# Optimization experiments

Hardware: AMD Instinct MI355X
Metric: run time of the kernel (lower is better)

Reference implementation:

```python
import jax, jax.numpy as jnp
import numpy as np
import math

B, T, C, H = 16384, 64, 48, 48


def setup_inputs() -> dict:
    key = jax.random.key(0)
    kx, kq, kk, kv = jax.random.split(key, 4)
    return {
        "x": jax.random.normal(kx, (B, T, C), dtype=jnp.float32),
        "Wq": jax.random.normal(kq, (C, H), dtype=jnp.float32) * 0.02,
        "Wk": jax.random.normal(kk, (C, H), dtype=jnp.float32) * 0.02,
        "Wv": jax.random.normal(kv, (C, H), dtype=jnp.float32) * 0.02,
    }


def reference(x, Wq, Wk, Wv):
    # x: [B, T, C]; projections (Linear with bias=False): [B, T, H]
    q = x @ Wq
    k = x @ Wk
    v = x @ Wv
    scale = 1.0 / math.sqrt(H)
    # scores: [B, T, T]
    wei = jnp.einsum("bth,bsh->bts", q, k) * scale
    causal = jnp.tril(jnp.ones((T, T), dtype=bool))  # tril mask, T==BLOCK_SIZE
    wei = jnp.where(causal, wei, -jnp.inf)
    wei = jax.nn.softmax(wei, axis=-1)
    # dropout is identity in eval mode
    return jnp.einsum("bts,bsh->bth", wei, v)
```

## Files before the change

kernel.cpp:

```cpp
#include <hip/hip_runtime.h>
#include <math.h>

typedef __bf16 bf16x8 __attribute__((ext_vector_type(8)));
typedef float f32x4 __attribute__((ext_vector_type(4)));
typedef unsigned short u16;

__device__ __forceinline__ u16 f2b(float f) {
  unsigned u = __builtin_bit_cast(unsigned, f);
  u = (u + 0x7fffu + ((u >> 16) & 1u)) >> 16;
  return (u16)u;
}

__device__ __forceinline__ f32x4 mfma16(bf16x8 a, bf16x8 b, f32x4 c) {
  return __builtin_amdgcn_mfma_f32_16x16x32_bf16(a, b, c, 0, 0, 0);
}

__device__ __forceinline__ int sw(int r, int c) {
  return (r << 6) + ((((c >> 3) ^ r) & 7) << 3) + (c & 7);
}
__device__ __forceinline__ int swc(int r, int ch) {
  return (r << 6) + (((ch ^ r) & 7) << 3);
}

__global__ __launch_bounds__(256) void head_prep(const float* __restrict__ Wq,
                                                 const float* __restrict__ Wk,
                                                 const float* __restrict__ Wv,
                                                 u16* __restrict__ ws) {
  __shared__ float wq[2304], wk[2304], wv[2304];
  const float scale = 0.14433756729740643f;
  for (int i = threadIdx.x; i < 2304; i += 256) {
    wq[i] = Wq[i];
    wk[i] = Wk[i];
    wv[i] = Wv[i];
  }
  __syncthreads();
  for (int idx = threadIdx.x; idx < 96 * 64; idx += 256) {
    int r = idx >> 6, c = idx & 63;
    float v = 0.f;
    if (c < 48) {
      if (r < 48) {
        float a = 0.f;
        for (int h = 0; h < 48; ++h) a += wq[c * 48 + h] * wk[r * 48 + h];
        v = a * scale;
      } else {
        v = wv[c * 48 + (r - 48)];
      }
    }
    ws[sw(r, c)] = f2b(v);
  }
}

__global__ __launch_bounds__(256, 6) void head_main(const float* __restrict__ x,
                                                    const u16* __restrict__ wimg,
                                                    float* __restrict__ out) {
  __shared__ u16 lds[208 * 64];
  u16* const R0 = lds;
  u16* const X  = lds + 96 * 64;
  u16* const VT = lds + 160 * 64;

  const int tid  = threadIdx.x;
  const int lane = tid & 63;
  const int w    = tid >> 6;
  const int qd   = lane >> 4;
  const int col  = lane & 15;
  const long b   = blockIdx.x;

  {
    const uint4* src = (const uint4*)wimg;
    uint4* dst = (uint4*)lds;
    dst[tid]       = src[tid];
    dst[tid + 256] = src[tid + 256];
    dst[tid + 512] = src[tid + 512];
  }
  {
    const float* xb = x + b * 3072 + w * 768;
#pragma unroll
    for (int it = 0; it < 3; ++it) {
      int e0 = lane * 4 + it * 256;
      float4 v = *(const float4*)(xb + e0);
      int row = 16 * w + e0 / 48;
      int c0  = e0 % 48;
      ushort4 pk;
      pk.x = f2b(v.x); pk.y = f2b(v.y); pk.z = f2b(v.z); pk.w = f2b(v.w);
      *(ushort4*)(X + sw(row, c0)) = pk;
    }
    ushort4 z = {0, 0, 0, 0};
    *(ushort4*)(X + sw(16 * w + col, 48 + 4 * qd)) = z;
  }
  __syncthreads();

  const int ar = 16 * w + col;
  const bf16x8 xa0 = *(const bf16x8*)(X + swc(ar, qd));
  const bf16x8 xa1 = *(const bf16x8*)(X + swc(ar, qd + 4));

  f32x4 aq[3];
#pragma unroll
  for (int n = 0; n < 3; ++n) {
    const int mr = 16 * n + col;
    const bf16x8 m0 = *(const bf16x8*)(R0 + swc(mr, qd));
    const bf16x8 m1 = *(const bf16x8*)(R0 + swc(mr, qd + 4));
    const bf16x8 v0 = *(const bf16x8*)(R0 + swc(48 + mr, qd));
    const bf16x8 v1 = *(const bf16x8*)(R0 + swc(48 + mr, qd + 4));
    f32x4 a = {0.f, 0.f, 0.f, 0.f};
    a = mfma16(m0, xa0, a);
    a = mfma16(m1, xa1, a);
    aq[n] = a;
    f32x4 av = {0.f, 0.f, 0.f, 0.f};
    av = mfma16(xa0, v0, av);
    av = mfma16(xa1, v1, av);
    ushort4 pv;
    pv.x = f2b(av[0]); pv.y = f2b(av[1]); pv.z = f2b(av[2]); pv.w = f2b(av[3]);
    *(ushort4*)(VT + sw(16 * n + col, 16 * w + 4 * qd)) = pv;
  }

  __syncthreads();

#pragma unroll
  for (int n = 0; n < 3; ++n) {
    ushort4 pq;
    pq.x = f2b(aq[n][0]); pq.y = f2b(aq[n][1]);
    pq.z = f2b(aq[n][2]); pq.w = f2b(aq[n][3]);
    *(ushort4*)(R0 + sw(16 * w + col, 16 * n + 4 * qd)) = pq;
  }
  __threadfence_block();

  float sv[4][4];
  {
    const bf16x8 qb0 = *(const bf16x8*)(R0 + swc(ar, qd));
    const bf16x8 qb1 = *(const bf16x8*)(R0 + swc(ar, qd + 4));
#pragma unroll
    for (int st = 0; st < 4; ++st) {
      const int br = 16 * st + col;
      f32x4 a = {0.f, 0.f, 0.f, 0.f};
      a = mfma16(*(const bf16x8*)(X + swc(br, qd)), qb0, a);
      a = mfma16(*(const bf16x8*)(X + swc(br, qd + 4)), qb1, a);
#pragma unroll
      for (int i = 0; i < 4; ++i) sv[st][i] = a[i];
    }
  }

  const int tg = 16 * w + col;
  float m = -INFINITY;
#pragma unroll
  for (int st = 0; st < 4; ++st)
#pragma unroll
    for (int i = 0; i < 4; ++i) {
      int sg = 16 * st + 4 * qd + i;
      float v = (sg <= tg) ? sv[st][i] : -INFINITY;
      sv[st][i] = v;
      m = fmaxf(m, v);
    }
  m = fmaxf(m, __shfl_xor(m, 16, 64));
  m = fmaxf(m, __shfl_xor(m, 32, 64));
  float l = 0.f;
#pragma unroll
  for (int st = 0; st < 4; ++st)
#pragma unroll
    for (int i = 0; i < 4; ++i) {
      float p = __expf(sv[st][i] - m);
      sv[st][i] = p;
      l += p;
    }
  l += __shfl_xor(l, 16, 64);
  l += __shfl_xor(l, 32, 64);
  float rl = __builtin_amdgcn_rcpf(l);

#pragma unroll
  for (int st = 0; st < 4; ++st) {
    ushort4 pk;
    pk.x = f2b(sv[st][0]); pk.y = f2b(sv[st][1]);
    pk.z = f2b(sv[st][2]); pk.w = f2b(sv[st][3]);
    *(ushort4*)(R0 + sw(16 * w + col, 16 * st + 4 * qd)) = pk;
  }
  __threadfence_block();

  f32x4 o0 = {0.f, 0.f, 0.f, 0.f}, o1 = o0, o2 = o0;
#pragma unroll
  for (int kt = 0; kt < 2; ++kt) {
    const int ch = qd + 4 * kt;
    bf16x8 pa = *(const bf16x8*)(R0 + swc(ar, ch));
    o0 = mfma16(pa, *(const bf16x8*)(VT + swc(0  + col, ch)), o0);
    o1 = mfma16(pa, *(const bf16x8*)(VT + swc(16 + col, ch)), o1);
    o2 = mfma16(pa, *(const bf16x8*)(VT + swc(32 + col, ch)), o2);
  }

  float* ob = out + b * 3072 + (16 * w + 4 * qd) * 48 + col;
#pragma unroll
  for (int i = 0; i < 4; ++i) {
    float rli = __shfl(rl, 4 * qd + i, 64);
    ob[i * 48 +  0] = o0[i] * rli;
    ob[i * 48 + 16] = o1[i] * rli;
    ob[i * 48 + 32] = o2[i] * rli;
  }
}

extern "C" void kernel_launch(void* const* d_in, const int* in_sizes, int n_in,
                              void* d_out, int out_size, void* d_ws, size_t ws_size,
                              hipStream_t stream) {
  const float* x  = (const float*)d_in[0];
  const float* Wq = (const float*)d_in[1];
  const float* Wk = (const float*)d_in[2];
  const float* Wv = (const float*)d_in[3];
  u16* wimg = (u16*)d_ws;
  head_prep<<<1, 256, 0, stream>>>(Wq, Wk, Wv, wimg);
  head_main<<<16384, 256, 0, stream>>>(x, wimg, (float*)d_out);
}
```

Measured before the change: 342.9 us.

## Overlay LDS regions to shrink shared memory and raise occupancy to seven blocks

Reuses the weight-image LDS area for V-transpose and Q/P staging after the projections finish, cutting the LDS footprint from 208 to 176 rows. Launch bounds go from 6 to 7 blocks per CU. The V store is deferred until after a barrier, and an extra __syncthreads is added before the score computation. The added barrier and longer-lived av registers could hurt, and the register cap may cause spills.

Result: no change. 343.4 us (+0.2%).

```diff
diff --git a/kernel.cpp b/kernel.cpp
--- a/kernel.cpp
+++ b/kernel.cpp
@@ -50,13 +50,12 @@
   }
 }
 
-__global__ __launch_bounds__(256, 6) void head_main(const float* __restrict__ x,
+__global__ __launch_bounds__(256, 7) void head_main(const float* __restrict__ x,
                                                     const u16* __restrict__ wimg,
                                                     float* __restrict__ out) {
-  __shared__ u16 lds[208 * 64];
-  u16* const R0 = lds;
+  __shared__ u16 lds[176 * 64];
   u16* const X  = lds + 96 * 64;
-  u16* const VT = lds + 160 * 64;
+  u16* const VT = lds + 48 * 64;
 
   const int tid  = threadIdx.x;
   const int lane = tid & 63;
@@ -64,6 +63,8 @@
   const int qd   = lane >> 4;
   const int col  = lane & 15;
   const long b   = blockIdx.x;
+  const int t_own = 16 * w + col;
+  const int qrow  = (w < 3) ? t_own : 112 + t_own;
 
   {
     const uint4* src = (const uint4*)wimg;
@@ -85,34 +86,31 @@
       *(ushort4*)(X + sw(row, c0)) = pk;
     }
     ushort4 z = {0, 0, 0, 0};
-    *(ushort4*)(X + sw(16 * w + col, 48 + 4 * qd)) = z;
-  }
-  __syncthreads();
-
-  const int ar = 16 * w + col;
-  const bf16x8 xa0 = *(const bf16x8*)(X + swc(ar, qd));
-  const bf16x8 xa1 = *(const bf16x8*)(X + swc(ar, qd + 4));
-
-  f32x4 aq[3];
+    *(ushort4*)(X + sw(t_own, 48 + 4 * qd)) = z;
+    if (w == 3) *(ushort4*)(lds + sw(160 + col, 48 + 4 * qd)) = z;
+  }
+  __syncthreads();
+
+  const bf16x8 xa0 = *(const bf16x8*)(X + swc(t_own, qd));
+  const bf16x8 xa1 = *(const bf16x8*)(X + swc(t_own, qd + 4));
+
+  f32x4 aq[3], av[3];
 #pragma unroll
   for (int n = 0; n < 3; ++n) {
     const int mr = 16 * n + col;
-    const bf16x8 m0 = *(const bf16x8*)(R0 + swc(mr, qd));
-    const bf16x8 m1 = *(const bf16x8*)(R0 + swc(mr, qd + 4));
-    const bf16x8 v0 = *(const bf16x8*)(R0 + swc(48 + mr, qd));
-    const bf16x8 v1 = *(const bf16x8*)(R0 + swc(48 + mr, qd + 4));
+    const bf16x8 m0 = *(const bf16x8*)(lds + swc(mr, qd));
+    const bf16x8 m1 = *(const bf16x8*)(lds + swc(mr, qd + 4));
+    const bf16x8 v0 = *(const bf16x8*)(lds + swc(48 + mr, qd));
+    const bf16x8 v1 = *(const bf16x8*)(lds + swc(48 + mr, qd + 4));
     f32x4 a = {0.f, 0.f, 0.f, 0.f};
     a = mfma16(m0, xa0, a);
     a = mfma16(m1, xa1, a);
     aq[n] = a;
-    f32x4 av = {0.f, 0.f, 0.f, 0.f};
-    av = mfma16(xa0, v0, av);
-    av = mfma16(xa1, v1, av);
-    ushort4 pv;
-    pv.x = f2b(av[0]); pv.y = f2b(av[1]); pv.z = f2b(av[2]); pv.w = f2b(av[3]);
-    *(ushort4*)(VT + sw(16 * n + col, 16 * w + 4 * qd)) = pv;
-  }
-
+    f32x4 c = {0.f, 0.f, 0.f, 0.f};
+    c = mfma16(xa0, v0, c);
+    c = mfma16(xa1, v1, c);
+    av[n] = c;
+  }
   __syncthreads();
 
 #pragma unroll
@@ -120,14 +118,18 @@
     ushort4 pq;
     pq.x = f2b(aq[n][0]); pq.y = f2b(aq[n][1]);
     pq.z = f2b(aq[n][2]); pq.w = f2b(aq[n][3]);
-    *(ushort4*)(R0 + sw(16 * w + col, 16 * n + 4 * qd)) = pq;
-  }
-  __threadfence_block();
+    *(ushort4*)(lds + sw(qrow, 16 * n + 4 * qd)) = pq;
+    ushort4 pv;
+    pv.x = f2b(av[n][0]); pv.y = f2b(av[n][1]);
+    pv.z = f2b(av[n][2]); pv.w = f2b(av[n][3]);
+    *(ushort4*)(VT + sw(16 * n + col, 16 * w + 4 * qd)) = pv;
+  }
+  __syncthreads();
 
   float sv[4][4];
   {
-    const bf16x8 qb0 = *(const bf16x8*)(R0 + swc(ar, qd));
-    const bf16x8 qb1 = *(const bf16x8*)(R0 + swc(ar, qd + 4));
+    const bf16x8 qb0 = *(const bf16x8*)(lds + swc(qrow, qd));
+    const bf16x8 qb1 = *(const bf16x8*)(lds + swc(qrow, qd + 4));
 #pragma unroll
     for (int st = 0; st < 4; ++st) {
       const int br = 16 * st + col;
@@ -139,14 +141,13 @@
     }
   }
 
-  const int tg = 16 * w + col;
   float m = -INFINITY;
 #pragma unroll
   for (int st = 0; st < 4; ++st)
 #pragma unroll
     for (int i = 0; i < 4; ++i) {
       int sg = 16 * st + 4 * qd + i;
-      float v = (sg <= tg) ? sv[st][i] : -INFINITY;
+      float v = (sg <= t_own) ? sv[st][i] : -INFINITY;
       sv[st][i] = v;
       m = fmaxf(m, v);
     }
@@ -170,7 +171,7 @@
     ushort4 pk;
     pk.x = f2b(sv[st][0]); pk.y = f2b(sv[st][1]);
     pk.z = f2b(sv[st][2]); pk.w = f2b(sv[st][3]);
-    *(ushort4*)(R0 + sw(16 * w + col, 16 * st + 4 * qd)) = pk;
+    *(ushort4*)(lds + sw(qrow, 16 * st + 4 * qd)) = pk;
   }
   __threadfence_block();
 
@@ -178,7 +179,7 @@
 #pragma unroll
   for (int kt = 0; kt < 2; ++kt) {
     const int ch = qd + 4 * kt;
-    bf16x8 pa = *(const bf16x8*)(R0 + swc(ar, ch));
+    bf16x8 pa = *(const bf16x8*)(lds + swc(qrow, ch));
     o0 = mfma16(pa, *(const bf16x8*)(VT + swc(0  + col, ch)), o0);
     o1 = mfma16(pa, *(const bf16x8*)(VT + swc(16 + col, ch)), o1);
     o2 = mfma16(pa, *(const bf16x8*)(VT + swc(32 + col, ch)), o2);
```
